# Optimization experiments

Hardware: AMD Instinct MI355X
Metric: run time of the kernel (lower is better)

The kernel has to match this reference:

```python
import jax, jax.numpy as jnp
import numpy as np

B = 8192          # batch size
OBS = 128         # observation dim
HID = 512         # input_size / hidden_size
HEADS = 4         # num_input_heads
VSZ = 256         # input_value_size
NU = 64           # num_units (rim_num)
K = 8             # top-k
NOPT = 16         # option_num


def setup_inputs() -> dict:
    key = jax.random.key(0)
    ks = jax.random.split(key, 8)
    return {
        "x": jax.random.normal(ks[0], (B, OBS), dtype=jnp.float32),
        "option": jax.random.randint(ks[1], (B,), 0, NOPT),
        "pre_fc_w": jax.random.normal(ks[2], (OBS, HID), dtype=jnp.float32) * (OBS ** -0.5),
        "pre_fc_b": jax.random.normal(ks[3], (HID,), dtype=jnp.float32) * 0.01,
        "value_w": jax.random.normal(ks[4], (HID, HEADS * VSZ), dtype=jnp.float32) * (HID ** -0.5),
        "value_b": jax.random.normal(ks[5], (HEADS * VSZ,), dtype=jnp.float32) * 0.01,
        "p_w": jax.random.normal(ks[6], (NOPT, NU), dtype=jnp.float32),
        "p_b": jax.random.normal(ks[7], (NU,), dtype=jnp.float32),
    }


def reference(x, option, pre_fc_w, pre_fc_b, value_w, value_b, p_w, p_b):
    b = x.shape[0]
    # pre_fc: [B, OBS] -> [B, HID]
    h = x @ pre_fc_w + pre_fc_b
    # concat null input slot -> [B, 2, HID]
    h2 = jnp.stack([h, jnp.zeros_like(h)], axis=1)
    # one-hot option + null slot -> [B, 2, NOPT]
    oh = jax.nn.one_hot(option, NOPT, dtype=jnp.float32)
    oh2 = jnp.stack([oh, jnp.zeros_like(oh)], axis=1)
    # value projection, split heads, mean over heads -> [B, 2, VSZ]
    v = (h2 @ value_w + value_b).reshape(b, 2, HEADS, VSZ)
    value_layer = jnp.mean(v, axis=2)
    # attention scores: einsum('bio,on->bni') -> [B, NU, 2]
    scores = jnp.einsum('bio,on->bni', oh2, p_w)
    # bias: p_b for real slot, zeros for null slot
    pb = jnp.stack([jnp.broadcast_to(p_b, (b, NU)), jnp.zeros((b, NU), jnp.float32)], axis=2)
    scores = scores + pb
    # top-k unit mask over not-null scores [B, NU]
    not_null = scores[:, :, 0]
    _, topk_idx = jax.lax.top_k(not_null, K)  # [B, K]
    mask = jnp.zeros((b, NU), jnp.float32).at[jnp.arange(b)[:, None], topk_idx].set(1.0)
    # softmax over the 2 slots (dropout is identity at eval)
    probs = jax.nn.softmax(scores, axis=-1)  # [B, NU, 2]
    # attention readout, masked, mean over units -> [B, VSZ]
    inputs = jnp.einsum('bns,bsv->bnv', probs, value_layer) * mask[:, :, None]
    return jnp.mean(inputs, axis=1)
```

## Files before the change

### kernel.cpp

```cpp
#include <hip/hip_runtime.h>
#include <hip/hip_bf16.h>

#define B_N   8192
#define OBS   128
#define HID   512
#define HEADS 4
#define VSZ   256
#define NU    64
#define TOPK  8
#define NOPT  16
#define KEXT  160

typedef __bf16 bf16_t;
typedef __bf16 bf16x8 __attribute__((ext_vector_type(8)));
typedef float  f32x4  __attribute__((ext_vector_type(4)));

#define OFF_WEFF 0u
#define OFF_A    524288u
#define OFF_DP   524352u
#define OFF_MT   525376u

__global__ void k_pre(const float* __restrict__ vw, const float* __restrict__ p_w,
                      const float* __restrict__ p_b, const float* __restrict__ vb,
                      float* __restrict__ weff, float* __restrict__ A,
                      float* __restrict__ Dp) {
    if (blockIdx.x < HID) {
        int j = blockIdx.x, v = threadIdx.x;
        const float* r = vw + j * (HEADS * VSZ);
        weff[j * VSZ + v] = 0.25f * (r[v] + r[v + VSZ] + r[v + 2 * VSZ] + r[v + 3 * VSZ]);
        return;
    }
    int tid  = threadIdx.x;
    int lane = tid & 63;
    int w    = tid >> 6;
    #pragma unroll
    for (int oo = 0; oo < 4; ++oo) {
        int o = w * 4 + oo;
        float cur = p_w[o * NU + lane] + p_b[lane];
        float sum = 0.f;
        #pragma unroll
        for (int t = 0; t < TOPK; ++t) {
            float m = cur;
            #pragma unroll
            for (int off = 32; off >= 1; off >>= 1)
                m = fmaxf(m, __shfl_xor(m, off));
            sum += 1.f / (1.f + expf(-m));
            unsigned long long bal = __ballot(cur == m);
            int first = __ffsll(bal) - 1;
            if (lane == first) cur = -1e30f;
        }
        if (lane == 0) A[o] = sum * (1.f / NU);
    }
    if (tid < VSZ)
        Dp[tid] = 0.125f * 0.25f * (vb[tid] + vb[tid + VSZ] + vb[tid + 2 * VSZ] + vb[tid + 3 * VSZ]);
}

__global__ void k_mt(const float* __restrict__ pw, const float* __restrict__ pb,
                     const float* __restrict__ weff, bf16_t* __restrict__ mt) {
    int k  = blockIdx.x;
    int v  = threadIdx.x & 255;
    int jq = threadIdx.x >> 8;
    __shared__ float red[1024];
    if (k > 128) {
        if (threadIdx.x < VSZ) mt[v * KEXT + k] = (bf16_t)0.f;
        return;
    }
    const float* wr = (k < OBS) ? (pw + k * HID) : pb;
    const float* wj = wr + jq * 128;
    const float* wf = weff + (jq * 128) * VSZ + v;
    float a0 = 0.f, a1 = 0.f, a2 = 0.f, a3 = 0.f;
    #pragma unroll 4
    for (int j = 0; j < 128; j += 4) {
        a0 += wj[j + 0] * wf[(j + 0) * VSZ];
        a1 += wj[j + 1] * wf[(j + 1) * VSZ];
        a2 += wj[j + 2] * wf[(j + 2) * VSZ];
        a3 += wj[j + 3] * wf[(j + 3) * VSZ];
    }
    red[threadIdx.x] = (a0 + a1) + (a2 + a3);
    __syncthreads();
    if (jq == 0) {
        float s = red[v] + red[v + 256] + red[v + 512] + red[v + 768];
        mt[v * KEXT + k] = (bf16_t)s;
    }
}

__launch_bounds__(256)
__global__ void k_main(const float* __restrict__ x, const bf16_t* __restrict__ mt,
                       const int* __restrict__ opt, const float* __restrict__ A,
                       const float* __restrict__ Dp, float* __restrict__ out) {
    int wave = threadIdx.x >> 6;
    int lane = threadIdx.x & 63;
    int mrow = lane & 15;
    int quad = lane >> 4;
    int r0   = blockIdx.x * 64 + wave * 16;
    int c0   = blockIdx.y * 128;

    f32x4 acc[8];
    #pragma unroll
    for (int t = 0; t < 8; ++t) acc[t] = (f32x4){0.f, 0.f, 0.f, 0.f};

    const float*  xr = x + (r0 + mrow) * OBS + quad * 8;
    const bf16_t* mb = mt + (c0 + mrow) * KEXT + quad * 8;

    #pragma unroll
    for (int kt = 0; kt < 5; ++kt) {
        bf16x8 a;
        if (kt < 4) {
            f32x4 lo = *(const f32x4*)(xr + kt * 32);
            f32x4 hi = *(const f32x4*)(xr + kt * 32 + 4);
            a[0] = (bf16_t)lo[0]; a[1] = (bf16_t)lo[1];
            a[2] = (bf16_t)lo[2]; a[3] = (bf16_t)lo[3];
            a[4] = (bf16_t)hi[0]; a[5] = (bf16_t)hi[1];
            a[6] = (bf16_t)hi[2]; a[7] = (bf16_t)hi[3];
        } else {
            #pragma unroll
            for (int j = 0; j < 8; ++j) a[j] = (bf16_t)0.f;
            if (quad == 0) a[0] = (bf16_t)1.0f;
        }
        #pragma unroll
        for (int t = 0; t < 8; ++t) {
            bf16x8 b = *(const bf16x8*)(mb + t * 16 * KEXT + kt * 32);
            acc[t] = __builtin_amdgcn_mfma_f32_16x16x32_bf16(a, b, acc[t], 0, 0, 0);
        }
    }

    #pragma unroll
    for (int r = 0; r < 4; ++r) {
        int row = r0 + quad * 4 + r;
        float av = A[opt[row]];
        float* orow = out + row * VSZ;
        #pragma unroll
        for (int t = 0; t < 8; ++t) {
            int col = c0 + t * 16 + mrow;
            orow[col] = av * acc[t][r] + Dp[col];
        }
    }
}

extern "C" void kernel_launch(void* const* d_in, const int* in_sizes, int n_in,
                              void* d_out, int out_size, void* d_ws, size_t ws_size,
                              hipStream_t stream) {
    const float* x        = (const float*)d_in[0];
    const int*   option   = (const int*)  d_in[1];
    const float* pre_fc_w = (const float*)d_in[2];
    const float* pre_fc_b = (const float*)d_in[3];
    const float* value_w  = (const float*)d_in[4];
    const float* value_b  = (const float*)d_in[5];
    const float* p_w      = (const float*)d_in[6];
    const float* p_b      = (const float*)d_in[7];
    float* out = (float*)d_out;

    char* ws = (char*)d_ws;
    float*  weff = (float*) (ws + OFF_WEFF);
    float*  A    = (float*) (ws + OFF_A);
    float*  Dp   = (float*) (ws + OFF_DP);
    bf16_t* mt   = (bf16_t*)(ws + OFF_MT);

    k_pre <<<dim3(HID + 1), dim3(VSZ), 0, stream>>>(value_w, p_w, p_b, value_b, weff, A, Dp);
    k_mt  <<<dim3(KEXT), dim3(1024), 0, stream>>>(pre_fc_w, pre_fc_b, weff, mt);
    k_main<<<dim3(B_N / 64, VSZ / 128), dim3(256), 0, stream>>>(x, mt, option, A, Dp, out);
}
```

Baseline: 97.60 us.

## Register-block k_mt over four K rows and halve k_main column tile

k_mt now computes four rows of the fused weight matrix per block, reusing each weff load across four accumulators and writing packed bf16x4. The bias row and zero padding are handled by one extra block, so the launch drops from 160 blocks to 33. k_main's column tile shrinks from 128 to 64, doubling the grid to 512 blocks for better CU occupancy, at the cost of loading x rows twice as often. The smaller k_mt grid reduces launch parallelism in exchange for more reuse per block.

```diff
diff --git a/kernel.cpp b/kernel.cpp
--- a/kernel.cpp
+++ b/kernel.cpp
@@ -12,6 +12,7 @@
 #define KEXT  160
 
 typedef __bf16 bf16_t;
+typedef __bf16 bf16x4 __attribute__((ext_vector_type(4)));
 typedef __bf16 bf16x8 __attribute__((ext_vector_type(8)));
 typedef float  f32x4  __attribute__((ext_vector_type(4)));
 
@@ -57,30 +58,50 @@
 
 __global__ void k_mt(const float* __restrict__ pw, const float* __restrict__ pb,
                      const float* __restrict__ weff, bf16_t* __restrict__ mt) {
-    int k  = blockIdx.x;
     int v  = threadIdx.x & 255;
     int jq = threadIdx.x >> 8;
-    __shared__ float red[1024];
-    if (k > 128) {
-        if (threadIdx.x < VSZ) mt[v * KEXT + k] = (bf16_t)0.f;
+    __shared__ float red[4][4][VSZ];
+    const float* wf = weff + (jq * 128) * VSZ + v;
+
+    if (blockIdx.x < 32) {
+        int k0 = blockIdx.x * 4;
+        const float* w0 = pw + (k0 + 0) * HID + jq * 128;
+        const float* w1 = pw + (k0 + 1) * HID + jq * 128;
+        const float* w2 = pw + (k0 + 2) * HID + jq * 128;
+        const float* w3 = pw + (k0 + 3) * HID + jq * 128;
+        float a0 = 0.f, a1 = 0.f, a2 = 0.f, a3 = 0.f;
+        #pragma unroll 8
+        for (int j = 0; j < 128; ++j) {
+            float wv = wf[j * VSZ];
+            a0 += w0[j] * wv;
+            a1 += w1[j] * wv;
+            a2 += w2[j] * wv;
+            a3 += w3[j] * wv;
+        }
+        red[jq][0][v] = a0; red[jq][1][v] = a1;
+        red[jq][2][v] = a2; red[jq][3][v] = a3;
+        __syncthreads();
+        if (jq == 0) {
+            bf16x4 o;
+            #pragma unroll
+            for (int t = 0; t < 4; ++t)
+                o[t] = (bf16_t)(red[0][t][v] + red[1][t][v] + red[2][t][v] + red[3][t][v]);
+            *(bf16x4*)(mt + v * KEXT + k0) = o;
+        }
         return;
     }
-    const float* wr = (k < OBS) ? (pw + k * HID) : pb;
-    const float* wj = wr + jq * 128;
-    const float* wf = weff + (jq * 128) * VSZ + v;
-    float a0 = 0.f, a1 = 0.f, a2 = 0.f, a3 = 0.f;
-    #pragma unroll 4
-    for (int j = 0; j < 128; j += 4) {
-        a0 += wj[j + 0] * wf[(j + 0) * VSZ];
-        a1 += wj[j + 1] * wf[(j + 1) * VSZ];
-        a2 += wj[j + 2] * wf[(j + 2) * VSZ];
-        a3 += wj[j + 3] * wf[(j + 3) * VSZ];
-    }
-    red[threadIdx.x] = (a0 + a1) + (a2 + a3);
+    const float* wr = pb + jq * 128;
+    float a0 = 0.f;
+    #pragma unroll 8
+    for (int j = 0; j < 128; ++j) a0 += wr[j] * wf[j * VSZ];
+    red[jq][0][v] = a0;
     __syncthreads();
     if (jq == 0) {
-        float s = red[v] + red[v + 256] + red[v + 512] + red[v + 768];
-        mt[v * KEXT + k] = (bf16_t)s;
+        float s = red[0][0][v] + red[1][0][v] + red[2][0][v] + red[3][0][v];
+        bf16_t* row = mt + v * KEXT;
+        row[128] = (bf16_t)s;
+        #pragma unroll
+        for (int k = 129; k < KEXT; ++k) row[k] = (bf16_t)0.f;
     }
 }
 
@@ -93,11 +114,11 @@
     int mrow = lane & 15;
     int quad = lane >> 4;
     int r0   = blockIdx.x * 64 + wave * 16;
-    int c0   = blockIdx.y * 128;
+    int c0   = blockIdx.y * 64;
 
-    f32x4 acc[8];
+    f32x4 acc[4];
     #pragma unroll
-    for (int t = 0; t < 8; ++t) acc[t] = (f32x4){0.f, 0.f, 0.f, 0.f};
+    for (int t = 0; t < 4; ++t) acc[t] = (f32x4){0.f, 0.f, 0.f, 0.f};
 
     const float*  xr = x + (r0 + mrow) * OBS + quad * 8;
     const bf16_t* mb = mt + (c0 + mrow) * KEXT + quad * 8;
@@ -118,7 +139,7 @@
             if (quad == 0) a[0] = (bf16_t)1.0f;
         }
         #pragma unroll
-        for (int t = 0; t < 8; ++t) {
+        for (int t = 0; t < 4; ++t) {
             bf16x8 b = *(const bf16x8*)(mb + t * 16 * KEXT + kt * 32);
             acc[t] = __builtin_amdgcn_mfma_f32_16x16x32_bf16(a, b, acc[t], 0, 0, 0);
         }
@@ -130,7 +151,7 @@
         float av = A[opt[row]];
         float* orow = out + row * VSZ;
         #pragma unroll
-        for (int t = 0; t < 8; ++t) {
+        for (int t = 0; t < 4; ++t) {
             int col = c0 + t * 16 + mrow;
             orow[col] = av * acc[t][r] + Dp[col];
         }
@@ -157,6 +178,6 @@
     bf16_t* mt   = (bf16_t*)(ws + OFF_MT);
 
     k_pre <<<dim3(HID + 1), dim3(VSZ), 0, stream>>>(value_w, p_w, p_b, value_b, weff, A, Dp);
-    k_mt  <<<dim3(KEXT), dim3(1024), 0, stream>>>(pre_fc_w, pre_fc_b, weff, mt);
-    k_main<<<dim3(B_N / 64, VSZ / 128), dim3(256), 0, stream>>>(x, mt, option, A, Dp, out);
+    k_mt  <<<dim3(33), dim3(1024), 0, stream>>>(pre_fc_w, pre_fc_b, weff, mt);
+    k_main<<<dim3(B_N / 64, VSZ / 64), dim3(256), 0, stream>>>(x, mt, option, A, Dp, out);
 }
```

New measurement: 108.1 us. 10.7% more time.

## Fuse three kernels into one persistent kernel with grid-wide atomic barriers

Applied to the files above, without the earlier changes.

Merges the preprocessing, weight-folding and main MFMA kernels into a single 128-block launch, using atomic-counter grid barriers between phases, with a memset to reset the counters. The weight-folding step is reorganised so each block computes two output columns via wave-level dot products over a transposed effective weight. The main phase now has each block cover both column halves of a 64-row tile and reuses the A fragments across them. This removes launch overhead and gaps between kernels, but it relies on all 128 blocks being co-resident and leaves only 128 blocks for the main GEMM phase.

```diff
diff --git a/kernel.cpp b/kernel.cpp
--- a/kernel.cpp
+++ b/kernel.cpp
@@ -4,135 +4,178 @@
 #define B_N   8192
 #define OBS   128
 #define HID   512
-#define HEADS 4
 #define VSZ   256
 #define NU    64
 #define TOPK  8
 #define NOPT  16
 #define KEXT  160
+#define NBLK  128
 
 typedef __bf16 bf16_t;
 typedef __bf16 bf16x8 __attribute__((ext_vector_type(8)));
 typedef float  f32x4  __attribute__((ext_vector_type(4)));
 
-#define OFF_WEFF 0u
-#define OFF_A    524288u
-#define OFF_DP   524352u
-#define OFF_MT   525376u
-
-__global__ void k_pre(const float* __restrict__ vw, const float* __restrict__ p_w,
-                      const float* __restrict__ p_b, const float* __restrict__ vb,
-                      float* __restrict__ weff, float* __restrict__ A,
-                      float* __restrict__ Dp) {
-    if (blockIdx.x < HID) {
-        int j = blockIdx.x, v = threadIdx.x;
-        const float* r = vw + j * (HEADS * VSZ);
-        weff[j * VSZ + v] = 0.25f * (r[v] + r[v + VSZ] + r[v + 2 * VSZ] + r[v + 3 * VSZ]);
-        return;
-    }
-    int tid  = threadIdx.x;
-    int lane = tid & 63;
-    int w    = tid >> 6;
-    #pragma unroll
-    for (int oo = 0; oo < 4; ++oo) {
-        int o = w * 4 + oo;
-        float cur = p_w[o * NU + lane] + p_b[lane];
-        float sum = 0.f;
-        #pragma unroll
-        for (int t = 0; t < TOPK; ++t) {
-            float m = cur;
-            #pragma unroll
-            for (int off = 32; off >= 1; off >>= 1)
-                m = fmaxf(m, __shfl_xor(m, off));
-            sum += 1.f / (1.f + expf(-m));
-            unsigned long long bal = __ballot(cur == m);
-            int first = __ffsll(bal) - 1;
-            if (lane == first) cur = -1e30f;
-        }
-        if (lane == 0) A[o] = sum * (1.f / NU);
-    }
-    if (tid < VSZ)
-        Dp[tid] = 0.125f * 0.25f * (vb[tid] + vb[tid + VSZ] + vb[tid + 2 * VSZ] + vb[tid + 3 * VSZ]);
+#define OFF_FLAGS 0u
+#define OFF_A     128u
+#define OFF_DP    256u
+#define OFF_WT    2048u
+#define OFF_MT    526336u
+
+__device__ __forceinline__ void gbar(unsigned* cnt) {
+    __syncthreads();
+    if (threadIdx.x == 0) {
+        __threadfence();
+        atomicAdd(cnt, 1u);
+        while (atomicAdd(cnt, 0u) < (unsigned)NBLK)
+            __builtin_amdgcn_s_sleep(1);
+        __threadfence();
+    }
+    __syncthreads();
 }
 
-__global__ void k_mt(const float* __restrict__ pw, const float* __restrict__ pb,
-                     const float* __restrict__ weff, bf16_t* __restrict__ mt) {
-    int k  = blockIdx.x;
-    int v  = threadIdx.x & 255;
-    int jq = threadIdx.x >> 8;
-    __shared__ float red[1024];
-    if (k > 128) {
-        if (threadIdx.x < VSZ) mt[v * KEXT + k] = (bf16_t)0.f;
-        return;
-    }
-    const float* wr = (k < OBS) ? (pw + k * HID) : pb;
-    const float* wj = wr + jq * 128;
-    const float* wf = weff + (jq * 128) * VSZ + v;
-    float a0 = 0.f, a1 = 0.f, a2 = 0.f, a3 = 0.f;
-    #pragma unroll 4
-    for (int j = 0; j < 128; j += 4) {
-        a0 += wj[j + 0] * wf[(j + 0) * VSZ];
-        a1 += wj[j + 1] * wf[(j + 1) * VSZ];
-        a2 += wj[j + 2] * wf[(j + 2) * VSZ];
-        a3 += wj[j + 3] * wf[(j + 3) * VSZ];
-    }
-    red[threadIdx.x] = (a0 + a1) + (a2 + a3);
-    __syncthreads();
-    if (jq == 0) {
-        float s = red[v] + red[v + 256] + red[v + 512] + red[v + 768];
-        mt[v * KEXT + k] = (bf16_t)s;
-    }
-}
-
 __launch_bounds__(256)
-__global__ void k_main(const float* __restrict__ x, const bf16_t* __restrict__ mt,
-                       const int* __restrict__ opt, const float* __restrict__ A,
-                       const float* __restrict__ Dp, float* __restrict__ out) {
-    int wave = threadIdx.x >> 6;
-    int lane = threadIdx.x & 63;
-    int mrow = lane & 15;
-    int quad = lane >> 4;
-    int r0   = blockIdx.x * 64 + wave * 16;
-    int c0   = blockIdx.y * 128;
-
-    f32x4 acc[8];
-    #pragma unroll
-    for (int t = 0; t < 8; ++t) acc[t] = (f32x4){0.f, 0.f, 0.f, 0.f};
-
-    const float*  xr = x + (r0 + mrow) * OBS + quad * 8;
-    const bf16_t* mb = mt + (c0 + mrow) * KEXT + quad * 8;
-
-    #pragma unroll
-    for (int kt = 0; kt < 5; ++kt) {
-        bf16x8 a;
-        if (kt < 4) {
+__global__ void k_fused(const float* __restrict__ x, const int* __restrict__ opt,
+                        const float* __restrict__ pw, const float* __restrict__ pb,
+                        const float* __restrict__ vw, const float* __restrict__ vb,
+                        const float* __restrict__ p_w, const float* __restrict__ p_b,
+                        float* __restrict__ out, char* __restrict__ ws) {
+    unsigned* flags = (unsigned*)(ws + OFF_FLAGS);
+    float*    A     = (float*)   (ws + OFF_A);
+    float*    Dp    = (float*)   (ws + OFF_DP);
+    float*    wefft = (float*)   (ws + OFF_WT);
+    bf16_t*   mt    = (bf16_t*)  (ws + OFF_MT);
+
+    const int tid  = threadIdx.x;
+    const int lane = tid & 63;
+    const int wv   = tid >> 6;
+
+    __shared__ float kbuf[2][132];
+
+    {
+        int j0 = blockIdx.x * 4;
+        float vals[4];
+        #pragma unroll
+        for (int jj = 0; jj < 4; ++jj) {
+            const float* r = vw + (j0 + jj) * (4 * VSZ);
+            vals[jj] = 0.25f * ((r[tid] + r[tid + 256]) + (r[tid + 512] + r[tid + 768]));
+        }
+        f32x4 o = {vals[0], vals[1], vals[2], vals[3]};
+        *(f32x4*)(wefft + tid * HID + j0) = o;
+
+        if (blockIdx.x == 0) {
+            #pragma unroll
+            for (int oo = 0; oo < 4; ++oo) {
+                int o_ = wv * 4 + oo;
+                float cur = p_w[o_ * NU + lane] + p_b[lane];
+                float sum = 0.f;
+                #pragma unroll
+                for (int t = 0; t < TOPK; ++t) {
+                    float m = cur;
+                    #pragma unroll
+                    for (int off = 32; off >= 1; off >>= 1)
+                        m = fmaxf(m, __shfl_xor(m, off));
+                    sum += 1.f / (1.f + expf(-m));
+                    unsigned long long bal = __ballot(cur == m);
+                    int first = __ffsll(bal) - 1;
+                    if (lane == first) cur = -1e30f;
+                }
+                if (lane == 0) A[o_] = sum * (1.f / NU);
+            }
+            Dp[tid] = 0.03125f * ((vb[tid] + vb[tid + 256]) + (vb[tid + 512] + vb[tid + 768]));
+        }
+    }
+    gbar(flags + 0);
+
+    {
+        int v0 = blockIdx.x * 2;
+        const float* wfp0 = wefft + v0 * HID + lane * 8;
+        const float* wfp1 = wfp0 + HID;
+        f32x4 w00 = *(const f32x4*)(wfp0),     w01 = *(const f32x4*)(wfp0 + 4);
+        f32x4 w10 = *(const f32x4*)(wfp1),     w11 = *(const f32x4*)(wfp1 + 4);
+
+        for (int it = 0; it < 33; ++it) {
+            if (it == 32 && wv != 0) break;
+            const float* pr = (it < 32) ? (pw + (wv * 32 + it) * HID + lane * 8)
+                                        : (pb + lane * 8);
+            f32x4 p0 = *(const f32x4*)(pr), p1 = *(const f32x4*)(pr + 4);
+            float s0 = ((p0[0]*w00[0] + p0[1]*w00[1]) + (p0[2]*w00[2] + p0[3]*w00[3]))
+                     + ((p1[0]*w01[0] + p1[1]*w01[1]) + (p1[2]*w01[2] + p1[3]*w01[3]));
+            float s1 = ((p0[0]*w10[0] + p0[1]*w10[1]) + (p0[2]*w10[2] + p0[3]*w10[3]))
+                     + ((p1[0]*w11[0] + p1[1]*w11[1]) + (p1[2]*w11[2] + p1[3]*w11[3]));
+            #pragma unroll
+            for (int off = 32; off >= 1; off >>= 1) {
+                s0 += __shfl_xor(s0, off);
+                s1 += __shfl_xor(s1, off);
+            }
+            if (lane == 0) {
+                int k = (it < 32) ? (wv * 32 + it) : 128;
+                kbuf[0][k] = s0;
+                kbuf[1][k] = s1;
+            }
+        }
+        __syncthreads();
+        #pragma unroll
+        for (int idx = tid; idx < 2 * KEXT; idx += 256) {
+            int vv = idx / KEXT;
+            int k  = idx - vv * KEXT;
+            float val = (k < 129) ? kbuf[vv][k] : 0.f;
+            mt[(v0 + vv) * KEXT + k] = (bf16_t)val;
+        }
+    }
+    gbar(flags + 1);
+
+    {
+        const int mrow = lane & 15;
+        const int quad = lane >> 4;
+        const int r0   = blockIdx.x * 64 + wv * 16;
+
+        bf16x8 af[5];
+        const float* xr = x + (r0 + mrow) * OBS + quad * 8;
+        #pragma unroll
+        for (int kt = 0; kt < 4; ++kt) {
             f32x4 lo = *(const f32x4*)(xr + kt * 32);
             f32x4 hi = *(const f32x4*)(xr + kt * 32 + 4);
+            bf16x8 a;
             a[0] = (bf16_t)lo[0]; a[1] = (bf16_t)lo[1];
             a[2] = (bf16_t)lo[2]; a[3] = (bf16_t)lo[3];
             a[4] = (bf16_t)hi[0]; a[5] = (bf16_t)hi[1];
             a[6] = (bf16_t)hi[2]; a[7] = (bf16_t)hi[3];
-        } else {
+            af[kt] = a;
+        }
+        {
+            bf16x8 a;
             #pragma unroll
             for (int j = 0; j < 8; ++j) a[j] = (bf16_t)0.f;
             if (quad == 0) a[0] = (bf16_t)1.0f;
-        }
-        #pragma unroll
-        for (int t = 0; t < 8; ++t) {
-            bf16x8 b = *(const bf16x8*)(mb + t * 16 * KEXT + kt * 32);
-            acc[t] = __builtin_amdgcn_mfma_f32_16x16x32_bf16(a, b, acc[t], 0, 0, 0);
-        }
-    }
-
-    #pragma unroll
-    for (int r = 0; r < 4; ++r) {
-        int row = r0 + quad * 4 + r;
-        float av = A[opt[row]];
-        float* orow = out + row * VSZ;
-        #pragma unroll
-        for (int t = 0; t < 8; ++t) {
-            int col = c0 + t * 16 + mrow;
-            orow[col] = av * acc[t][r] + Dp[col];
+            af[4] = a;
+        }
+
+        #pragma unroll
+        for (int half = 0; half < 2; ++half) {
+            int c0 = half * 128;
+            f32x4 acc[8];
+            #pragma unroll
+            for (int t = 0; t < 8; ++t) acc[t] = (f32x4){0.f, 0.f, 0.f, 0.f};
+            const bf16_t* mb = mt + (c0 + mrow) * KEXT + quad * 8;
+            #pragma unroll
+            for (int kt = 0; kt < 5; ++kt) {
+                #pragma unroll
+                for (int t = 0; t < 8; ++t) {
+                    bf16x8 b = *(const bf16x8*)(mb + t * 16 * KEXT + kt * 32);
+                    acc[t] = __builtin_amdgcn_mfma_f32_16x16x32_bf16(af[kt], b, acc[t], 0, 0, 0);
+                }
+            }
+            #pragma unroll
+            for (int r = 0; r < 4; ++r) {
+                int row = r0 + quad * 4 + r;
+                float av = A[opt[row]];
+                float* orow = out + row * VSZ;
+                #pragma unroll
+                for (int t = 0; t < 8; ++t) {
+                    int col = c0 + t * 16 + mrow;
+                    orow[col] = av * acc[t][r] + Dp[col];
+                }
+            }
         }
     }
 }
@@ -149,14 +192,10 @@
     const float* p_w      = (const float*)d_in[6];
     const float* p_b      = (const float*)d_in[7];
     float* out = (float*)d_out;
-
-    char* ws = (char*)d_ws;
-    float*  weff = (float*) (ws + OFF_WEFF);
-    float*  A    = (float*) (ws + OFF_A);
-    float*  Dp   = (float*) (ws + OFF_DP);
-    bf16_t* mt   = (bf16_t*)(ws + OFF_MT);
-
-    k_pre <<<dim3(HID + 1), dim3(VSZ), 0, stream>>>(value_w, p_w, p_b, value_b, weff, A, Dp);
-    k_mt  <<<dim3(KEXT), dim3(1024), 0, stream>>>(pre_fc_w, pre_fc_b, weff, mt);
-    k_main<<<dim3(B_N / 64, VSZ / 128), dim3(256), 0, stream>>>(x, mt, option, A, Dp, out);
+    char*  ws  = (char*)d_ws;
+
+    hipMemsetAsync(ws + OFF_FLAGS, 0, 8, stream);
+
+    k_fused<<<dim3(NBLK), dim3(256), 0, stream>>>(
+        x, option, pre_fc_w, pre_fc_b, value_w, value_b, p_w, p_b, out, ws);
 }
```

New measurement: 133.3 us. +36.6%, slower.
